# Performance work log

Hardware: AMD Instinct MI355X
Metric: run time of the kernel (lower is better)

## Reference

```python
import jax, jax.numpy as jnp
import numpy as np

EMBED_DIM = 768
NUM_HEADS = 12
HEAD_SIZE = EMBED_DIM // NUM_HEADS


def setup_inputs() -> dict:
    key = jax.random.key(0)
    ks = jax.random.split(key, 9)
    B, S, D = 4, 2048, EMBED_DIM
    scale = 1.0 / np.sqrt(D)
    x = jax.random.normal(ks[0], (B, S, D), dtype=jnp.float32)
    # Linear params (torch nn.Linear: y = x @ W.T + b); store W as [in, out] for einsum
    Wq = jax.random.normal(ks[1], (D, D), dtype=jnp.float32) * scale
    bq = jnp.zeros((D,), dtype=jnp.float32)
    Wk = jax.random.normal(ks[2], (D, D), dtype=jnp.float32) * scale
    bk = jnp.zeros((D,), dtype=jnp.float32)
    Wv = jax.random.normal(ks[3], (D, D), dtype=jnp.float32) * scale
    bv = jnp.zeros((D,), dtype=jnp.float32)
    Wo = jax.random.normal(ks[4], (D, D), dtype=jnp.float32) * scale
    bo = jnp.zeros((D,), dtype=jnp.float32)
    return {"x": x, "Wq": Wq, "bq": bq, "Wk": Wk, "bk": bk,
            "Wv": Wv, "bv": bv, "Wo": Wo, "bo": bo}


def reference(x, Wq, bq, Wk, bk, Wv, bv, Wo, bo):
    B, S, D = x.shape
    H, hs = NUM_HEADS, HEAD_SIZE
    scale = hs ** (-0.5)
    # Projections
    Q = (x @ Wq + bq).reshape(B, S, H, hs)
    K = (x @ Wk + bk).reshape(B, S, H, hs)
    V = (x @ Wv + bv).reshape(B, S, H, hs)
    # Batched attention over all heads (equivalent to the per-head loop:
    # torch view splits last dim into H contiguous chunks; concat of per-head
    # outputs along -1 restores the same layout)
    scores = jnp.einsum('bqhd,bkhd->bhqk', Q, K) * scale  # [B,H,S,S]
    attn = jax.nn.softmax(scores, axis=-1)
    out = jnp.einsum('bhqk,bkhd->bqhd', attn, V).reshape(B, S, D)
    # Output projection; dropout is identity in eval mode
    return out @ Wo + bo
```

## Files before the change

kernel.cpp:

```cpp
#include <hip/hip_runtime.h>

typedef unsigned short ushort_t;
typedef __bf16 bf16x8 __attribute__((ext_vector_type(8)));
typedef float floatx4 __attribute__((ext_vector_type(4)));

__device__ inline ushort_t f2bf(float f) {
    __bf16 h = (__bf16)f;
    return __builtin_bit_cast(ushort_t, h);
}

__device__ inline void gload16(const void* g, void* l) {
    __builtin_amdgcn_global_load_lds((const __attribute__((address_space(1))) void*)g,
                                     (__attribute__((address_space(3))) void*)l, 16, 0, 0);
}

__global__ __launch_bounds__(256) void prep_kernel(
    const float* __restrict__ x, ushort_t* __restrict__ xbf,
    const float* __restrict__ W0, const float* __restrict__ W1,
    const float* __restrict__ W2, const float* __restrict__ W3,
    ushort_t* __restrict__ T0, ushort_t* __restrict__ T1,
    ushort_t* __restrict__ T2, ushort_t* __restrict__ T3) {
    int bx = blockIdx.x;
    int tid = threadIdx.x;
    if (bx < 2304) {
        __shared__ float t[32][33];
        int w = bx / 576, rem = bx % 576;
        const float* W; ushort_t* T;
        switch (w) {
            case 0: W = W0; T = T0; break;
            case 1: W = W1; T = T1; break;
            case 2: W = W2; T = T2; break;
            default: W = W3; T = T3; break;
        }
        int n0 = (rem / 24) * 32, k0 = (rem % 24) * 32;
        int tx = tid & 31, ty = tid >> 5;
        for (int i = 0; i < 4; ++i)
            t[ty + i * 8][tx] = W[(k0 + ty + i * 8) * 768 + n0 + tx];
        __syncthreads();
        for (int i = 0; i < 4; ++i)
            T[(n0 + ty + i * 8) * 768 + k0 + tx] = f2bf(t[tx][ty + i * 8]);
    } else {
        int i = ((bx - 2304) * 256 + tid) * 4;
        float4 v = *(const float4*)(x + i);
        ushort4 u;
        u.x = f2bf(v.x); u.y = f2bf(v.y); u.z = f2bf(v.z); u.w = f2bf(v.w);
        *(ushort4*)(xbf + i) = u;
    }
}

__global__ __launch_bounds__(256) void gemm_qkv(
    const ushort_t* __restrict__ A,
    const ushort_t* __restrict__ Tq, const ushort_t* __restrict__ Tk, const ushort_t* __restrict__ Tv,
    const float* __restrict__ bq, const float* __restrict__ bk, const float* __restrict__ bv,
    ushort_t* __restrict__ Qb, ushort_t* __restrict__ Kb, ushort_t* __restrict__ Vtb) {
    __shared__ ushort_t sh[128 * 64 + 64 * 64];
    ushort_t* As = sh;
    ushort_t* Bs = sh + 128 * 64;
    int tid = threadIdx.x;
    int bid = blockIdx.x;
    int xcd = bid & 7;
    int idx = bid >> 3;
    int bx = xcd * 8 + (idx & 7);
    int by = idx >> 3;
    int m0 = bx * 128;
    int which = by / 12;
    int n0 = (by % 12) * 64;
    const ushort_t* Bt = which == 0 ? Tq : (which == 1 ? Tk : Tv);
    const float* bias = which == 0 ? bq : (which == 1 ? bk : bv);

    int wave = tid >> 6;
    int lane = tid & 63;
    int ln = tid & 15;
    int quad = (tid >> 4) & 3;
    int wm = wave * 32;
    int lr = lane >> 3;
    int lc = (lane & 7) * 8;

    floatx4 acc[2][4];
    floatx4 z = {0.f, 0.f, 0.f, 0.f};
    for (int i = 0; i < 2; ++i)
        for (int j = 0; j < 4; ++j) acc[i][j] = z;

    for (int kt = 0; kt < 12; ++kt) {
        int k0 = kt * 64;
        __syncthreads();
        for (int i = 0; i < 4; ++i) {
            int c = wave * 4 + i;
            gload16(&A[(m0 + c * 8 + lr) * 768 + k0 + lc], &As[c * 512]);
        }
        for (int i = 0; i < 2; ++i) {
            int c = wave * 2 + i;
            gload16(&Bt[(n0 + c * 8 + lr) * 768 + k0 + lc], &Bs[c * 512]);
        }
        __syncthreads();
        for (int ks = 0; ks < 2; ++ks) {
            bf16x8 a[2], b[4];
            for (int i = 0; i < 2; ++i)
                a[i] = *(const bf16x8*)&As[(wm + i * 16 + ln) * 64 + ks * 32 + quad * 8];
            for (int j = 0; j < 4; ++j)
                b[j] = *(const bf16x8*)&Bs[(j * 16 + ln) * 64 + ks * 32 + quad * 8];
            for (int i = 0; i < 2; ++i)
                for (int j = 0; j < 4; ++j)
                    acc[i][j] = __builtin_amdgcn_mfma_f32_16x16x32_bf16(a[i], b[j], acc[i][j], 0, 0, 0);
        }
    }

    const float QSCALE = 0.125f * 1.44269504088896f;
    if (which != 2) {
        for (int i = 0; i < 2; ++i) {
            for (int j = 0; j < 4; ++j) {
                int gn = n0 + j * 16 + ln;
                float bia = bias[gn];
                int h = gn >> 6, dd = gn & 63;
                for (int r = 0; r < 4; ++r) {
                    int gm = m0 + wm + i * 16 + quad * 4 + r;
                    int bb = gm >> 11, ss = gm & 2047;
                    float v = acc[i][j][r] + bia;
                    if (which == 0) {
                        Qb[((bb * 12 + h) * 2048 + ss) * 64 + dd] = f2bf(v * QSCALE);
                    } else {
                        Kb[((bb * 12 + h) * 2048 + ss) * 64 + dd] = f2bf(v);
                    }
                }
            }
        }
    } else {
        __syncthreads();
        ushort_t* tr = sh;
        for (int j = 0; j < 4; ++j) {
            int nl = j * 16 + ln;
            float bia = bias[n0 + nl];
            for (int i = 0; i < 2; ++i) {
                ushort4 u;
                u.x = f2bf(acc[i][j][0] + bia);
                u.y = f2bf(acc[i][j][1] + bia);
                u.z = f2bf(acc[i][j][2] + bia);
                u.w = f2bf(acc[i][j][3] + bia);
                *(ushort4*)&tr[nl * 136 + wm + i * 16 + quad * 4] = u;
            }
        }
        __syncthreads();
        int bb = m0 >> 11, ss0 = m0 & 2047;
        int head = by % 12;
        for (int p = 0; p < 4; ++p) {
            int n = p * 16 + (tid >> 4);
            int mc = (tid & 15) * 8;
            uint4 v = *(const uint4*)&tr[n * 136 + mc];
            *(uint4*)&Vtb[(size_t)((bb * 12 + head) * 64 + n) * 2048 + ss0 + mc] = v;
        }
    }
}

__global__ __launch_bounds__(256, 2) void attn_kernel(
    const ushort_t* __restrict__ Qb, const ushort_t* __restrict__ Kb,
    const ushort_t* __restrict__ Vtb, ushort_t* __restrict__ Ob) {
    __shared__ ushort_t Vs[2][64 * 72];
    int tid = threadIdx.x;
    int bid = blockIdx.x;
    int swz = (bid & 7) * 96 + (bid >> 3);
    int bh = swz >> 4;
    int qt = swz & 15;
    int wave = tid >> 6;
    int qh = wave >> 1;
    int kh = wave & 1;
    int ln = tid & 15;
    int quad = (tid >> 4) & 3;
    int q0 = qt * 128 + qh * 64;

    const ushort_t* Qp = Qb + (size_t)bh * 2048 * 64;
    const ushort_t* Kp = Kb + (size_t)bh * 2048 * 64;
    const ushort_t* Vp = Vtb + (size_t)bh * 64 * 2048;

    bf16x8 bqf[4][2];
    for (int g = 0; g < 4; ++g)
        for (int ks = 0; ks < 2; ++ks)
            bqf[g][ks] = *(const bf16x8*)&Qp[(q0 + g * 16 + ln) * 64 + ks * 32 + quad * 8];

    int srow = tid >> 3;
    int c8 = tid & 7;
    int scol = c8 * 8;
    int u = c8 & 3;
    int vcol = (c8 >> 2) * 32 + (u & 1) * 16 + (u >> 1) * 4;

    uint4 vreg[2];

    for (int p = 0; p < 2; ++p)
        vreg[p] = *(const uint4*)&Vp[(p * 32 + srow) * 2048 + scol];
    for (int p = 0; p < 2; ++p) {
        ushort_t* vb = &Vs[0][(p * 32 + srow) * 72 + vcol];
        *(uint2*)vb = make_uint2(vreg[p].x, vreg[p].y);
        *(uint2*)(vb + 8) = make_uint2(vreg[p].z, vreg[p].w);
    }
    bf16x8 akc[2][2];
    for (int m = 0; m < 2; ++m)
        for (int ks = 0; ks < 2; ++ks)
            akc[m][ks] = *(const bf16x8*)&Kp[((kh * 2 + m) * 16 + ln) * 64 + ks * 32 + quad * 8];
    __syncthreads();

    floatx4 o_acc[4][4];
    float lsum[4] = {0.f, 0.f, 0.f, 0.f};
    floatx4 z = {0.f, 0.f, 0.f, 0.f};
    for (int g = 0; g < 4; ++g)
        for (int m4 = 0; m4 < 4; ++m4) o_acc[g][m4] = z;

    for (int kt = 0; kt < 32; ++kt) {
        int cur = kt & 1;
        bf16x8 akn[2][2];
        if (kt < 31) {
            for (int p = 0; p < 2; ++p)
                vreg[p] = *(const uint4*)&Vp[(p * 32 + srow) * 2048 + (kt + 1) * 64 + scol];
            for (int m = 0; m < 2; ++m)
                for (int ks = 0; ks < 2; ++ks)
                    akn[m][ks] = *(const bf16x8*)&Kp[((kt + 1) * 64 + (kh * 2 + m) * 16 + ln) * 64 + ks * 32 + quad * 8];
        }

        const ushort_t* VsH = Vs[cur];

        floatx4 st[4][2];
        for (int g = 0; g < 4; ++g)
            for (int m = 0; m < 2; ++m) {
                floatx4 s = z;
                s = __builtin_amdgcn_mfma_f32_16x16x32_bf16(akc[m][0], bqf[g][0], s, 0, 0, 0);
                s = __builtin_amdgcn_mfma_f32_16x16x32_bf16(akc[m][1], bqf[g][1], s, 0, 0, 0);
                st[g][m] = s;
            }

        for (int g = 0; g < 4; ++g)
            for (int m = 0; m < 2; ++m)
                for (int r = 0; r < 4; ++r) {
                    float e = __builtin_amdgcn_exp2f(st[g][m][r]);
                    st[g][m][r] = e;
                    lsum[g] += e;
                }

        bf16x8 av[4];
        for (int m4 = 0; m4 < 4; ++m4)
            av[m4] = *(const bf16x8*)&VsH[(m4 * 16 + ln) * 72 + kh * 32 + quad * 8];

        for (int g = 0; g < 4; ++g) {
            bf16x8 b;
            b[0] = (__bf16)st[g][0][0];
            b[1] = (__bf16)st[g][0][1];
            b[2] = (__bf16)st[g][0][2];
            b[3] = (__bf16)st[g][0][3];
            b[4] = (__bf16)st[g][1][0];
            b[5] = (__bf16)st[g][1][1];
            b[6] = (__bf16)st[g][1][2];
            b[7] = (__bf16)st[g][1][3];
            for (int m4 = 0; m4 < 4; ++m4)
                o_acc[g][m4] = __builtin_amdgcn_mfma_f32_16x16x32_bf16(av[m4], b, o_acc[g][m4], 0, 0, 0);
        }

        if (kt < 31) {
            int nxt = cur ^ 1;
            for (int p = 0; p < 2; ++p) {
                ushort_t* vb = &Vs[nxt][(p * 32 + srow) * 72 + vcol];
                *(uint2*)vb = make_uint2(vreg[p].x, vreg[p].y);
                *(uint2*)(vb + 8) = make_uint2(vreg[p].z, vreg[p].w);
            }
            for (int m = 0; m < 2; ++m)
                for (int ks = 0; ks < 2; ++ks)
                    akc[m][ks] = akn[m][ks];
        }
        __syncthreads();
    }

    for (int g = 0; g < 4; ++g) {
        lsum[g] += __shfl_xor(lsum[g], 16);
        lsum[g] += __shfl_xor(lsum[g], 32);
    }

    float* mbuf = (float*)&Vs[0][0];
    float* lbuf = mbuf + 64 * 68;
    int b = bh / 12, h = bh % 12;
    for (int ph = 0; ph < 2; ++ph) {
        if (kh == 1 && qh == ph) {
            for (int g = 0; g < 4; ++g) {
                for (int m4 = 0; m4 < 4; ++m4)
                    *(floatx4*)&mbuf[(g * 16 + ln) * 68 + m4 * 16 + quad * 4] = o_acc[g][m4];
                if (quad == 0) lbuf[g * 16 + ln] = lsum[g];
            }
        }
        __syncthreads();
        if (kh == 0 && qh == ph) {
            for (int g = 0; g < 4; ++g) {
                float inv = 1.f / (lsum[g] + lbuf[g * 16 + ln]);
                int token = b * 2048 + q0 + g * 16 + ln;
                for (int m4 = 0; m4 < 4; ++m4) {
                    floatx4 o2 = *(const floatx4*)&mbuf[(g * 16 + ln) * 68 + m4 * 16 + quad * 4];
                    for (int r = 0; r < 4; ++r)
                        Ob[token * 768 + h * 64 + m4 * 16 + quad * 4 + r] =
                            f2bf((o_acc[g][m4][r] + o2[r]) * inv);
                }
            }
        }
        __syncthreads();
    }
}

__global__ __launch_bounds__(256) void gemm_out(
    const ushort_t* __restrict__ A, const ushort_t* __restrict__ Bt,
    const float* __restrict__ bias, float* __restrict__ out) {
    __shared__ ushort_t As[128 * 64];
    __shared__ ushort_t Bs[64 * 64];
    int tid = threadIdx.x;
    int m0 = blockIdx.x * 128;
    int n0 = blockIdx.y * 64;

    int wave = tid >> 6;
    int lane = tid & 63;
    int ln = tid & 15;
    int quad = (tid >> 4) & 3;
    int wm = wave * 32;
    int lr = lane >> 3;
    int lc = (lane & 7) * 8;

    floatx4 acc[2][4];
    floatx4 z = {0.f, 0.f, 0.f, 0.f};
    for (int i = 0; i < 2; ++i)
        for (int j = 0; j < 4; ++j) acc[i][j] = z;

    for (int kt = 0; kt < 12; ++kt) {
        int k0 = kt * 64;
        __syncthreads();
        for (int i = 0; i < 4; ++i) {
            int c = wave * 4 + i;
            gload16(&A[(m0 + c * 8 + lr) * 768 + k0 + lc], &As[c * 512]);
        }
        for (int i = 0; i < 2; ++i) {
            int c = wave * 2 + i;
            gload16(&Bt[(n0 + c * 8 + lr) * 768 + k0 + lc], &Bs[c * 512]);
        }
        __syncthreads();
        for (int ks = 0; ks < 2; ++ks) {
            bf16x8 a[2], b[4];
            for (int i = 0; i < 2; ++i)
                a[i] = *(const bf16x8*)&As[(wm + i * 16 + ln) * 64 + ks * 32 + quad * 8];
            for (int j = 0; j < 4; ++j)
                b[j] = *(const bf16x8*)&Bs[(j * 16 + ln) * 64 + ks * 32 + quad * 8];
            for (int i = 0; i < 2; ++i)
                for (int j = 0; j < 4; ++j)
                    acc[i][j] = __builtin_amdgcn_mfma_f32_16x16x32_bf16(a[i], b[j], acc[i][j], 0, 0, 0);
        }
    }

    for (int i = 0; i < 2; ++i) {
        for (int j = 0; j < 4; ++j) {
            int gn = n0 + j * 16 + ln;
            float bia = bias[gn];
            for (int r = 0; r < 4; ++r) {
                int gm = m0 + wm + i * 16 + quad * 4 + r;
                out[gm * 768 + gn] = acc[i][j][r] + bia;
            }
        }
    }
}

extern "C" void kernel_launch(void* const* d_in, const int* in_sizes, int n_in,
                              void* d_out, int out_size, void* d_ws, size_t ws_size,
                              hipStream_t stream) {
    const float* x  = (const float*)d_in[0];
    const float* Wq = (const float*)d_in[1];
    const float* bq = (const float*)d_in[2];
    const float* Wk = (const float*)d_in[3];
    const float* bk = (const float*)d_in[4];
    const float* Wv = (const float*)d_in[5];
    const float* bv = (const float*)d_in[6];
    const float* Wo = (const float*)d_in[7];
    const float* bo = (const float*)d_in[8];

    const int NTOK = 4 * 2048;
    const int NELT = NTOK * 768;
    const int WELT = 768 * 768;

    ushort_t* xbf = (ushort_t*)d_ws;
    ushort_t* Tq  = xbf + NELT;
    ushort_t* Tk  = Tq + WELT;
    ushort_t* Tv  = Tk + WELT;
    ushort_t* To  = Tv + WELT;
    ushort_t* Qb  = To + WELT;
    ushort_t* Kb  = Qb + NELT;
    ushort_t* Vtb = Kb + NELT;
    ushort_t* Ob  = Vtb + NELT;

    prep_kernel<<<8448, 256, 0, stream>>>(x, xbf, Wq, Wk, Wv, Wo, Tq, Tk, Tv, To);
    gemm_qkv<<<2304, 256, 0, stream>>>(xbf, Tq, Tk, Tv, bq, bk, bv, Qb, Kb, Vtb);
    attn_kernel<<<768, 256, 0, stream>>>(Qb, Kb, Vtb, Ob);
    gemm_out<<<dim3(64, 12), 256, 0, stream>>>(Ob, To, bo, (float*)d_out);
}
```

Baseline: 239.7 us.

## Stage K tiles through swizzled LDS with async global-to-LDS loads in attention

Result: faster. 226.7 us (-5.4%).

```diff
diff --git a/kernel.cpp b/kernel.cpp
--- a/kernel.cpp
+++ b/kernel.cpp
@@ -57,12 +57,8 @@
     ushort_t* As = sh;
     ushort_t* Bs = sh + 128 * 64;
     int tid = threadIdx.x;
-    int bid = blockIdx.x;
-    int xcd = bid & 7;
-    int idx = bid >> 3;
-    int bx = xcd * 8 + (idx & 7);
-    int by = idx >> 3;
-    int m0 = bx * 128;
+    int m0 = blockIdx.x * 128;
+    int by = blockIdx.y;
     int which = by / 12;
     int n0 = (by % 12) * 64;
     const ushort_t* Bt = which == 0 ? Tq : (which == 1 ? Tk : Tv);
@@ -119,7 +115,7 @@
                     if (which == 0) {
                         Qb[((bb * 12 + h) * 2048 + ss) * 64 + dd] = f2bf(v * QSCALE);
                     } else {
-                        Kb[((bb * 12 + h) * 2048 + ss) * 64 + dd] = f2bf(v);
+                        Kb[((bb * 12 + h) * 2048 + ss) * 64 + (dd ^ ((ss & 7) << 3))] = f2bf(v);
                     }
                 }
             }
@@ -154,6 +150,7 @@
 __global__ __launch_bounds__(256, 2) void attn_kernel(
     const ushort_t* __restrict__ Qb, const ushort_t* __restrict__ Kb,
     const ushort_t* __restrict__ Vtb, ushort_t* __restrict__ Ob) {
+    __shared__ ushort_t Ks[2][64 * 64];
     __shared__ ushort_t Vs[2][64 * 72];
     int tid = threadIdx.x;
     int bid = blockIdx.x;
@@ -163,6 +160,7 @@
     int wave = tid >> 6;
     int qh = wave >> 1;
     int kh = wave & 1;
+    int lane = tid & 63;
     int ln = tid & 15;
     int quad = (tid >> 4) & 3;
     int q0 = qt * 128 + qh * 64;
@@ -176,6 +174,8 @@
         for (int ks = 0; ks < 2; ++ks)
             bqf[g][ks] = *(const bf16x8*)&Qp[(q0 + g * 16 + ln) * 64 + ks * 32 + quad * 8];
 
+    int lr = lane >> 3;
+    int lc = (lane & 7) * 8;
     int srow = tid >> 3;
     int c8 = tid & 7;
     int scol = c8 * 8;
@@ -184,6 +184,10 @@
 
     uint4 vreg[2];
 
+    for (int i = 0; i < 2; ++i) {
+        int c = wave * 2 + i;
+        gload16(&Kp[(c * 8 + lr) * 64 + lc], &Ks[0][c * 512]);
+    }
     for (int p = 0; p < 2; ++p)
         vreg[p] = *(const uint4*)&Vp[(p * 32 + srow) * 2048 + scol];
     for (int p = 0; p < 2; ++p) {
@@ -191,10 +195,6 @@
         *(uint2*)vb = make_uint2(vreg[p].x, vreg[p].y);
         *(uint2*)(vb + 8) = make_uint2(vreg[p].z, vreg[p].w);
     }
-    bf16x8 akc[2][2];
-    for (int m = 0; m < 2; ++m)
-        for (int ks = 0; ks < 2; ++ks)
-            akc[m][ks] = *(const bf16x8*)&Kp[((kh * 2 + m) * 16 + ln) * 64 + ks * 32 + quad * 8];
     __syncthreads();
 
     floatx4 o_acc[4][4];
@@ -205,23 +205,33 @@
 
     for (int kt = 0; kt < 32; ++kt) {
         int cur = kt & 1;
-        bf16x8 akn[2][2];
         if (kt < 31) {
+            int nxt = cur ^ 1;
+            for (int i = 0; i < 2; ++i) {
+                int c = wave * 2 + i;
+                gload16(&Kp[((kt + 1) * 64 + c * 8 + lr) * 64 + lc], &Ks[nxt][c * 512]);
+            }
             for (int p = 0; p < 2; ++p)
                 vreg[p] = *(const uint4*)&Vp[(p * 32 + srow) * 2048 + (kt + 1) * 64 + scol];
-            for (int m = 0; m < 2; ++m)
-                for (int ks = 0; ks < 2; ++ks)
-                    akn[m][ks] = *(const bf16x8*)&Kp[((kt + 1) * 64 + (kh * 2 + m) * 16 + ln) * 64 + ks * 32 + quad * 8];
-        }
-
+        }
+
+        const ushort_t* KsH = Ks[cur];
         const ushort_t* VsH = Vs[cur];
+
+        bf16x8 ak[2][2];
+        for (int m = 0; m < 2; ++m) {
+            int row = (kh * 2 + m) * 16 + ln;
+            int xr = (ln & 7) << 3;
+            for (int ks = 0; ks < 2; ++ks)
+                ak[m][ks] = *(const bf16x8*)&KsH[row * 64 + ((ks * 32 + quad * 8) ^ xr)];
+        }
 
         floatx4 st[4][2];
         for (int g = 0; g < 4; ++g)
             for (int m = 0; m < 2; ++m) {
                 floatx4 s = z;
-                s = __builtin_amdgcn_mfma_f32_16x16x32_bf16(akc[m][0], bqf[g][0], s, 0, 0, 0);
-                s = __builtin_amdgcn_mfma_f32_16x16x32_bf16(akc[m][1], bqf[g][1], s, 0, 0, 0);
+                s = __builtin_amdgcn_mfma_f32_16x16x32_bf16(ak[m][0], bqf[g][0], s, 0, 0, 0);
+                s = __builtin_amdgcn_mfma_f32_16x16x32_bf16(ak[m][1], bqf[g][1], s, 0, 0, 0);
                 st[g][m] = s;
             }
 
@@ -258,9 +268,6 @@
                 *(uint2*)vb = make_uint2(vreg[p].x, vreg[p].y);
                 *(uint2*)(vb + 8) = make_uint2(vreg[p].z, vreg[p].w);
             }
-            for (int m = 0; m < 2; ++m)
-                for (int ks = 0; ks < 2; ++ks)
-                    akc[m][ks] = akn[m][ks];
         }
         __syncthreads();
     }
@@ -384,7 +391,7 @@
     ushort_t* Ob  = Vtb + NELT;
 
     prep_kernel<<<8448, 256, 0, stream>>>(x, xbf, Wq, Wk, Wv, Wo, Tq, Tk, Tv, To);
-    gemm_qkv<<<2304, 256, 0, stream>>>(xbf, Tq, Tk, Tv, bq, bk, bv, Qb, Kb, Vtb);
+    gemm_qkv<<<dim3(64, 36), 256, 0, stream>>>(xbf, Tq, Tk, Tv, bq, bk, bv, Qb, Kb, Vtb);
     attn_kernel<<<768, 256, 0, stream>>>(Qb, Kb, Vtb, Ob);
     gemm_out<<<dim3(64, 12), 256, 0, stream>>>(Ob, To, bo, (float*)d_out);
 }
```
